# Performance work log

Measured on AMD Instinct MI355X. Metric: run time of the kernel, lower is better.

Reference implementation:

```python
import jax, jax.numpy as jnp
import numpy as np

B, S, D, H = 2, 2048, 2048, 16
HD = D // H  # head_dim = 128


def setup_inputs() -> dict:
    key = jax.random.key(0)
    ks = jax.random.split(key, 10)
    sc = 1.0 / np.sqrt(D)
    inp = {
        "hidden_states": jax.random.normal(ks[0], (B, S, D), dtype=jnp.float32),
        "attention_mask": jnp.zeros((B, 1, S, S), dtype=jnp.float32),
        "Wq": jax.random.normal(ks[1], (D, D), dtype=jnp.float32) * sc,
        "bq": jnp.zeros((D,), dtype=jnp.float32),
        "Wk": jax.random.normal(ks[2], (D, D), dtype=jnp.float32) * sc,
        "bk": jnp.zeros((D,), dtype=jnp.float32),
        "Wv": jax.random.normal(ks[3], (D, D), dtype=jnp.float32) * sc,
        "bv": jnp.zeros((D,), dtype=jnp.float32),
        "Wo": jax.random.normal(ks[4], (D, D), dtype=jnp.float32) * sc,
        "bo": jnp.zeros((D,), dtype=jnp.float32),
    }
    return inp


def reference(hidden_states, attention_mask, Wq, bq, Wk, bk, Wv, bv, Wo, bo):
    # torch Linear: y = x @ W^T + b
    q = hidden_states @ Wq.T + bq
    k = hidden_states @ Wk.T + bk
    v = hidden_states @ Wv.T + bv
    # [B,S,D] -> [B,H,S,HD]
    q = q.reshape(B, S, H, HD).transpose(0, 2, 1, 3)
    k = k.reshape(B, S, H, HD).transpose(0, 2, 1, 3)
    v = v.reshape(B, S, H, HD).transpose(0, 2, 1, 3)
    # RoPE in source is an identity passthrough; apply_rotary_pos_emb returns (q, k) unchanged.
    scores = jnp.einsum("bhqd,bhkd->bhqk", q, k) / jnp.sqrt(jnp.float32(HD))
    scores = scores + attention_mask  # broadcast over heads
    attn = jax.nn.softmax(scores, axis=-1)
    out = jnp.einsum("bhqk,bhkd->bhqd", attn, v)
    out = out.transpose(0, 2, 1, 3).reshape(B, S, D)
    return out @ Wo.T + bo
```

## Files before the change

### kernel.cpp

```cpp
#include <hip/hip_runtime.h>
#include <hip/hip_bf16.h>
#include <math.h>

typedef unsigned short u16;
typedef unsigned int u32;
typedef __attribute__((ext_vector_type(8))) short bf16x8;
typedef __attribute__((ext_vector_type(4))) float f32x4;

constexpr int Bc = 2, Sc = 2048, Dc = 2048, Hc = 16, HDc = 128;
constexpr int Mc = Bc * Sc;
constexpr float SCALE = 0.08838834764831845f;
constexpr float LOG2E = 1.4426950408889634f;

__device__ inline u16 f2bf(float f) {
  __hip_bfloat16 h = __float2bfloat16(f);
  return __builtin_bit_cast(u16, h);
}

typedef const __attribute__((address_space(1))) u32 glb_u32;
typedef __attribute__((address_space(3))) u32 lds_u32;
__device__ inline void gload16(const void* g, void* l) {
  __builtin_amdgcn_global_load_lds((glb_u32*)g, (lds_u32*)l, 16, 0, 0);
}

__global__ __launch_bounds__(256) void cvt5(
    const float* __restrict__ s0, u16* __restrict__ d0, int n0,
    const float* __restrict__ s1, u16* __restrict__ d1, int n1,
    const float* __restrict__ s2, u16* __restrict__ d2, int n2,
    const float* __restrict__ s3, u16* __restrict__ d3, int n3,
    const float* __restrict__ s4, u16* __restrict__ d4, int n4) {
  int i = blockIdx.x * 256 + threadIdx.x;
  const float* s; u16* d;
  if (i < n0) { s = s0; d = d0; }
  else { i -= n0;
    if (i < n1) { s = s1; d = d1; }
    else { i -= n1;
      if (i < n2) { s = s2; d = d2; }
      else { i -= n2;
        if (i < n3) { s = s3; d = d3; }
        else { i -= n3;
          if (i >= n4) return;
          s = s4; d = d4; } } } }
  float4 v = reinterpret_cast<const float4*>(s)[i];
  ushort4 o;
  o.x = f2bf(v.x); o.y = f2bf(v.y); o.z = f2bf(v.z); o.w = f2bf(v.w);
  reinterpret_cast<ushort4*>(d)[i] = o;
}

__global__ __launch_bounds__(512, 2) void qk_gemm8(
    const u16* __restrict__ A, const u16* __restrict__ Wq,
    const u16* __restrict__ Wk, const float* __restrict__ bq,
    const float* __restrict__ bk, u16* __restrict__ qout,
    u16* __restrict__ kout) {
  __shared__ u16 lds[65536];
  char* L = (char*)lds;
  const int t = threadIdx.x, w = t >> 6, lane = t & 63, g = lane >> 4, c = lane & 15;
  const int wm = w >> 2, wn = w & 3;
  const int m0 = blockIdx.y * 256, n0 = blockIdx.x * 256;
  const int z = blockIdx.z;
  const u16* W = z ? Wk : Wq;
  const float* bias = z ? bk : bq;
  const float scale = z ? 1.0f : SCALE * LOG2E;

  f32x4 acc[8][4];
#pragma unroll
  for (int m = 0; m < 8; ++m)
#pragma unroll
    for (int n = 0; n < 4; ++n) acc[m][n] = 0.f;

  const u16* sPtr[8];
  int dOff[8];
#pragma unroll
  for (int i = 0; i < 8; ++i) {
    int i2 = i & 3;
    int u = i2 * 512 + t;
    int row = u >> 3, p = u & 7;
    int cu = (p ^ row) & 7;
    const u16* base = (i < 4) ? (A + (size_t)(m0 + row) * Dc)
                              : (W + (size_t)(n0 + row) * Dc);
    sPtr[i] = base + cu * 8;
    dOff[i] = ((i >= 4) ? 32768 : 0) + (i2 >> 1) * 16384 +
              ((i2 & 1) * 512 + (t & 448)) * 16;
  }

  auto STAGE = [&](int d) {
#pragma unroll
    for (int i = 0; i < 8; ++i) {
      gload16(sPtr[i], L + d * 65536 + dOff[i]);
      sPtr[i] += 64;
    }
  };

  STAGE(0);
  asm volatile("s_waitcnt vmcnt(0)" ::: "memory");
  asm volatile("s_barrier" ::: "memory");

  int cur = 0;
  const char* AbBase = L + wm * 16384;
  const char* BbBase = L + 32768 + (wn >> 1) * 16384;
  const int rB0 = (wn & 1) * 64;

#pragma unroll 1
  for (int s = 0; s < 32; ++s) {
    if (s + 1 < 32) {
      STAGE(cur ^ 1);
      asm volatile("s_waitcnt vmcnt(8)" ::: "memory");
    } else {
      asm volatile("s_waitcnt vmcnt(0)" ::: "memory");
    }
    asm volatile("s_barrier" ::: "memory");

    const char* Ab = AbBase + cur * 65536;
    const char* Bb = BbBase + cur * 65536;
#pragma unroll
    for (int mh = 0; mh < 2; ++mh)
#pragma unroll
      for (int ks = 0; ks < 2; ++ks) {
        bf16x8 af[4], bf[4];
#pragma unroll
        for (int m4 = 0; m4 < 4; ++m4) {
          int row = (mh * 4 + m4) * 16 + c;
          af[m4] = *(const bf16x8*)(Ab + row * 128 + (((ks * 4 + g) ^ row) & 7) * 16);
        }
#pragma unroll
        for (int n = 0; n < 4; ++n) {
          int row = rB0 + n * 16 + c;
          bf[n] = *(const bf16x8*)(Bb + row * 128 + (((ks * 4 + g) ^ row) & 7) * 16);
        }
        __builtin_amdgcn_s_setprio(1);
#pragma unroll
        for (int m4 = 0; m4 < 4; ++m4)
#pragma unroll
          for (int n = 0; n < 4; ++n)
            acc[mh * 4 + m4][n] =
                __builtin_amdgcn_mfma_f32_16x16x32_bf16(af[m4], bf[n], acc[mh * 4 + m4][n], 0, 0, 0);
        __builtin_amdgcn_s_setprio(0);
      }

    asm volatile("s_barrier" ::: "memory");
    cur ^= 1;
  }

  u16* outp = z ? kout : qout;
#pragma unroll
  for (int n = 0; n < 4; ++n) {
    int col = n0 + wn * 64 + n * 16 + c;
    float bvv = bias[col];
    int h = col >> 7, d = col & (HDc - 1);
#pragma unroll
    for (int m = 0; m < 8; ++m)
#pragma unroll
      for (int r = 0; r < 4; ++r) {
        int row = m0 + wm * 128 + m * 16 + g * 4 + r;
        int b = row >> 11, si = row & (Sc - 1);
        outp[((size_t)((b * Hc + h) * Sc + si)) * HDc + d] =
            f2bf((acc[m][n][r] + bvv) * scale);
      }
  }
}

constexpr int GBM = 128, GBN = 128, GBK = 64;

__global__ __launch_bounds__(256) void v_gemm(
    const u16* __restrict__ A, const u16* __restrict__ W,
    const float* __restrict__ bias, u16* __restrict__ vout) {
  __shared__ u16 smem[17408];
  u16* As = smem;
  u16* Bs = smem + 8192;
  char* Asb = (char*)As;
  char* Bsb = (char*)Bs;
  const int t = threadIdx.x;
  const int w = t >> 6, lane = t & 63, g = lane >> 4, c = lane & 15;
  const int wm = w >> 1, wn = w & 1;
  const int m0 = blockIdx.y * GBM, n0 = blockIdx.x * GBN;

  f32x4 acc[4][4];
#pragma unroll
  for (int m = 0; m < 4; ++m)
#pragma unroll
    for (int n = 0; n < 4; ++n) acc[m][n] = 0.f;

  for (int k0 = 0; k0 < Dc; k0 += GBK) {
#pragma unroll
    for (int i = 0; i < 4; ++i) {
      int u = i * 256 + t;
      int row = u >> 3, p = u & 7;
      int cu = (p ^ row) & 7;
      int ub = i * 256 + (t & 192);
      gload16(A + (size_t)(m0 + row) * Dc + k0 + cu * 8, Asb + ub * 16);
      gload16(W + (size_t)(n0 + row) * Dc + k0 + cu * 8, Bsb + ub * 16);
    }
    __syncthreads();
#pragma unroll
    for (int s = 0; s < 2; ++s) {
      bf16x8 af[4], bfv[4];
#pragma unroll
      for (int m = 0; m < 4; ++m) {
        int row = wm * 64 + m * 16 + c;
        int scu = ((s * 4 + g) ^ row) & 7;
        af[m] = *(const bf16x8*)(Asb + row * 128 + scu * 16);
      }
#pragma unroll
      for (int n = 0; n < 4; ++n) {
        int row = wn * 64 + n * 16 + c;
        int scu = ((s * 4 + g) ^ row) & 7;
        bfv[n] = *(const bf16x8*)(Bsb + row * 128 + scu * 16);
      }
#pragma unroll
      for (int m = 0; m < 4; ++m)
#pragma unroll
        for (int n = 0; n < 4; ++n)
          acc[m][n] = __builtin_amdgcn_mfma_f32_16x16x32_bf16(af[m], bfv[n], acc[m][n], 0, 0, 0);
    }
    __syncthreads();
  }

  u16* CT = smem;
  __syncthreads();
#pragma unroll
  for (int m = 0; m < 4; ++m)
#pragma unroll
    for (int n = 0; n < 4; ++n) {
      int lcol = wn * 64 + n * 16 + c;
      float bvv = bias[n0 + lcol];
#pragma unroll
      for (int r = 0; r < 4; ++r) {
        int lrow = wm * 64 + m * 16 + g * 4 + r;
        CT[lcol * 136 + lrow] = f2bf(acc[m][n][r] + bvv);
      }
    }
  __syncthreads();
  const int b = m0 >> 11, h = n0 >> 7, s0 = m0 & (Sc - 1);
#pragma unroll
  for (int i = 0; i < 8; ++i) {
    int u = i * 256 + t;
    int d = u >> 4, su = u & 15;
    size_t gbase = ((size_t)((b * Hc + h) * HDc) + d) * Sc + s0;
#pragma unroll
    for (int p2 = 0; p2 < 4; ++p2) {
      int sl = su * 8 + p2 * 2;
      u32 val = (u32)CT[d * 136 + sl] | ((u32)CT[d * 136 + sl + 1] << 16);
      int w6 = sl & 63, blk = sl >> 6;
      int slot = ((w6 >> 5) << 5) | (((w6 >> 2) & 3) << 3) |
                 (((w6 >> 4) & 1) << 2) | (w6 & 3);
      *(u32*)&vout[gbase + blk * 64 + slot] = val;
    }
  }
}

__global__ __launch_bounds__(256) void gemm_out(
    const u16* __restrict__ A, const u16* __restrict__ W,
    const float* __restrict__ bias, float* __restrict__ outp) {
  __shared__ u16 smem[16384];
  u16* As = smem;
  u16* Bs = smem + 8192;
  char* Asb = (char*)As;
  char* Bsb = (char*)Bs;
  const int t = threadIdx.x;
  const int w = t >> 6, lane = t & 63, g = lane >> 4, c = lane & 15;
  const int wm = w >> 1, wn = w & 1;
  const int m0 = blockIdx.y * GBM, n0 = blockIdx.x * GBN;

  f32x4 acc[4][4];
#pragma unroll
  for (int m = 0; m < 4; ++m)
#pragma unroll
    for (int n = 0; n < 4; ++n) acc[m][n] = 0.f;

  for (int k0 = 0; k0 < Dc; k0 += GBK) {
#pragma unroll
    for (int i = 0; i < 4; ++i) {
      int u = i * 256 + t;
      int row = u >> 3, p = u & 7;
      int cu = (p ^ row) & 7;
      int ub = i * 256 + (t & 192);
      gload16(A + (size_t)(m0 + row) * Dc + k0 + cu * 8, Asb + ub * 16);
      gload16(W + (size_t)(n0 + row) * Dc + k0 + cu * 8, Bsb + ub * 16);
    }
    __syncthreads();
#pragma unroll
    for (int s = 0; s < 2; ++s) {
      bf16x8 af[4], bfv[4];
#pragma unroll
      for (int m = 0; m < 4; ++m) {
        int row = wm * 64 + m * 16 + c;
        int scu = ((s * 4 + g) ^ row) & 7;
        af[m] = *(const bf16x8*)(Asb + row * 128 + scu * 16);
      }
#pragma unroll
      for (int n = 0; n < 4; ++n) {
        int row = wn * 64 + n * 16 + c;
        int scu = ((s * 4 + g) ^ row) & 7;
        bfv[n] = *(const bf16x8*)(Bsb + row * 128 + scu * 16);
      }
#pragma unroll
      for (int m = 0; m < 4; ++m)
#pragma unroll
        for (int n = 0; n < 4; ++n)
          acc[m][n] = __builtin_amdgcn_mfma_f32_16x16x32_bf16(af[m], bfv[n], acc[m][n], 0, 0, 0);
    }
    __syncthreads();
  }

#pragma unroll
  for (int m = 0; m < 4; ++m)
#pragma unroll
    for (int n = 0; n < 4; ++n) {
      int col = n0 + wn * 64 + n * 16 + c;
      float bv = bias[col];
#pragma unroll
      for (int r = 0; r < 4; ++r) {
        int row = m0 + wm * 64 + m * 16 + g * 4 + r;
        outp[(size_t)row * Dc + col] = acc[m][n][r] + bv;
      }
    }
}

__global__ __launch_bounds__(128, 2) void attn_mfma(
    const u16* __restrict__ Q, const u16* __restrict__ K,
    const u16* __restrict__ VT, const float* __restrict__ mask,
    u16* __restrict__ outb) {
  __shared__ u16 Ks[64 * 128];
  __shared__ u16 Vt[128 * 64];
  char* Ksb = (char*)Ks;
  char* Vtb = (char*)Vt;
  const int t = threadIdx.x, w = t >> 6, lane = t & 63, g = lane >> 4, c = lane & 15;
  const int bid = blockIdx.x;
  const int nid = (bid & 7) * 128 + (bid >> 3);
  const int bh = nid >> 5;
  const int q0 = (nid & 31) * 64;
  const int bq = bh >> 4, h = bh & 15;
  const u16* Qp = Q + ((size_t)bh << 18);
  const u16* Kp = K + ((size_t)bh << 18);
  const u16* VTp = VT + ((size_t)bh << 18);

  bf16x8 qf0[4], qf1[4];
  {
    int qr0 = q0 + w * 32 + c;
#pragma unroll
    for (int d0 = 0; d0 < 4; ++d0) {
      qf0[d0] = *(const bf16x8*)(Qp + (size_t)qr0 * HDc + d0 * 32 + g * 8);
      qf1[d0] = *(const bf16x8*)(Qp + (size_t)(qr0 + 16) * HDc + d0 * 32 + g * 8);
    }
  }

  f32x4 po0[8], po1[8];
#pragma unroll
  for (int m = 0; m < 8; ++m) { po0[m] = 0.f; po1[m] = 0.f; }
  float lsum0 = 0.f, lsum1 = 0.f;
  const float* mrow0 = mask + ((size_t)bq * Sc + q0 + w * 32 + c) * Sc;
  const float* mrow1 = mrow0 + (size_t)16 * Sc;

#pragma unroll 1
  for (int kt = 0; kt < 32; ++kt) {
    const int k0 = kt * 64;
#pragma unroll
    for (int i = 0; i < 8; ++i) {
      int u = i * 128 + t, row = u >> 4, p = u & 15;
      int cu = (p & 8) | ((p ^ row) & 7);
      gload16(Kp + (size_t)(k0 + row) * HDc + cu * 8,
              Ksb + (i * 128 + (t & 64)) * 16);
    }
#pragma unroll
    for (int i = 0; i < 8; ++i) {
      int u = i * 128 + t, d = u >> 3, p = u & 7;
      int cu = (p ^ d) & 7;
      gload16(VTp + (size_t)d * Sc + k0 + cu * 8,
              Vtb + (i * 128 + (t & 64)) * 16);
    }
    float4 mk0[4], mk1[4];
#pragma unroll
    for (int n = 0; n < 4; ++n) {
      mk0[n] = *(const float4*)(mrow0 + k0 + n * 16 + g * 4);
      mk1[n] = *(const float4*)(mrow1 + k0 + n * 16 + g * 4);
    }
    __syncthreads();

    f32x4 sfr0[4], sfr1[4];
#pragma unroll
    for (int n = 0; n < 4; ++n) { sfr0[n] = 0.f; sfr1[n] = 0.f; }
    __builtin_amdgcn_s_setprio(1);
#pragma unroll
    for (int ds = 0; ds < 4; ++ds)
#pragma unroll
      for (int n = 0; n < 4; ++n) {
        int row = n * 16 + c;
        int cu = ds * 4 + g;
        int scu = (cu & 8) | ((cu ^ row) & 7);
        bf16x8 kf = *(const bf16x8*)(Ksb + row * 256 + scu * 16);
        sfr0[n] = __builtin_amdgcn_mfma_f32_16x16x32_bf16(kf, qf0[ds], sfr0[n], 0, 0, 0);
        sfr1[n] = __builtin_amdgcn_mfma_f32_16x16x32_bf16(kf, qf1[ds], sfr1[n], 0, 0, 0);
      }
    __builtin_amdgcn_s_setprio(0);

    u32 a01[4], a23[4], b01[4], b23[4];
#pragma unroll
    for (int n = 0; n < 4; ++n) {
      float p0 = __builtin_amdgcn_exp2f(fmaf(mk0[n].x, LOG2E, sfr0[n][0]));
      float p1 = __builtin_amdgcn_exp2f(fmaf(mk0[n].y, LOG2E, sfr0[n][1]));
      float p2 = __builtin_amdgcn_exp2f(fmaf(mk0[n].z, LOG2E, sfr0[n][2]));
      float p3 = __builtin_amdgcn_exp2f(fmaf(mk0[n].w, LOG2E, sfr0[n][3]));
      lsum0 += (p0 + p1) + (p2 + p3);
      a01[n] = (u32)f2bf(p0) | ((u32)f2bf(p1) << 16);
      a23[n] = (u32)f2bf(p2) | ((u32)f2bf(p3) << 16);
      float r0 = __builtin_amdgcn_exp2f(fmaf(mk1[n].x, LOG2E, sfr1[n][0]));
      float r1 = __builtin_amdgcn_exp2f(fmaf(mk1[n].y, LOG2E, sfr1[n][1]));
      float r2 = __builtin_amdgcn_exp2f(fmaf(mk1[n].z, LOG2E, sfr1[n][2]));
      float r3 = __builtin_amdgcn_exp2f(fmaf(mk1[n].w, LOG2E, sfr1[n][3]));
      lsum1 += (r0 + r1) + (r2 + r3);
      b01[n] = (u32)f2bf(r0) | ((u32)f2bf(r1) << 16);
      b23[n] = (u32)f2bf(r2) | ((u32)f2bf(r3) << 16);
    }

    __builtin_amdgcn_s_setprio(1);
#pragma unroll
    for (int s2 = 0; s2 < 2; ++s2) {
      uint4 pw0, pw1;
      pw0.x = a01[s2 * 2]; pw0.y = a23[s2 * 2];
      pw0.z = a01[s2 * 2 + 1]; pw0.w = a23[s2 * 2 + 1];
      pw1.x = b01[s2 * 2]; pw1.y = b23[s2 * 2];
      pw1.z = b01[s2 * 2 + 1]; pw1.w = b23[s2 * 2 + 1];
      bf16x8 pf0 = __builtin_bit_cast(bf16x8, pw0);
      bf16x8 pf1 = __builtin_bit_cast(bf16x8, pw1);
#pragma unroll
      for (int m = 0; m < 8; ++m) {
        int d = m * 16 + c;
        int scuv = ((s2 * 4 + g) ^ (d & 7)) & 7;
        bf16x8 vf = *(const bf16x8*)(Vtb + d * 128 + scuv * 16);
        po0[m] = __builtin_amdgcn_mfma_f32_16x16x32_bf16(vf, pf0, po0[m], 0, 0, 0);
        po1[m] = __builtin_amdgcn_mfma_f32_16x16x32_bf16(vf, pf1, po1[m], 0, 0, 0);
      }
    }
    __builtin_amdgcn_s_setprio(0);
    __syncthreads();
  }

  lsum0 += __shfl_xor(lsum0, 16, 64);
  lsum0 += __shfl_xor(lsum0, 32, 64);
  lsum1 += __shfl_xor(lsum1, 16, 64);
  lsum1 += __shfl_xor(lsum1, 32, 64);
  const float rl0 = 1.0f / lsum0;
  const float rl1 = 1.0f / lsum1;
  const int qg0 = q0 + w * 32 + c;
  u16* ob0 = outb + ((size_t)(bq * Sc + qg0)) * Dc + h * HDc;
  u16* ob1 = ob0 + (size_t)16 * Dc;
#pragma unroll
  for (int m = 0; m < 8; ++m) {
    ushort4 o4;
    o4.x = f2bf(po0[m][0] * rl0);
    o4.y = f2bf(po0[m][1] * rl0);
    o4.z = f2bf(po0[m][2] * rl0);
    o4.w = f2bf(po0[m][3] * rl0);
    *(ushort4*)(ob0 + m * 16 + g * 4) = o4;
    ushort4 o5;
    o5.x = f2bf(po1[m][0] * rl1);
    o5.y = f2bf(po1[m][1] * rl1);
    o5.z = f2bf(po1[m][2] * rl1);
    o5.w = f2bf(po1[m][3] * rl1);
    *(ushort4*)(ob1 + m * 16 + g * 4) = o5;
  }
}

extern "C" void kernel_launch(void* const* d_in, const int* in_sizes, int n_in,
                              void* d_out, int out_size, void* d_ws,
                              size_t ws_size, hipStream_t stream) {
  const float* hs   = (const float*)d_in[0];
  const float* mask = (const float*)d_in[1];
  const float* Wq   = (const float*)d_in[2];
  const float* bqp  = (const float*)d_in[3];
  const float* Wk   = (const float*)d_in[4];
  const float* bkp  = (const float*)d_in[5];
  const float* Wv   = (const float*)d_in[6];
  const float* bvp  = (const float*)d_in[7];
  const float* Wo   = (const float*)d_in[8];
  const float* bop  = (const float*)d_in[9];

  u16* Xb  = (u16*)d_ws;
  u16* Wqb = Xb + (size_t)Mc * Dc;
  u16* Wkb = Wqb + (size_t)Dc * Dc;
  u16* Wvb = Wkb + (size_t)Dc * Dc;
  u16* Wob = Wvb + (size_t)Dc * Dc;
  u16* qb  = Wob + (size_t)Dc * Dc;
  u16* kb  = qb + (size_t)Mc * Dc;
  u16* vtb = kb + (size_t)Mc * Dc;
  u16* ab  = vtb + (size_t)Mc * Dc;

  const int nh4 = Mc * Dc / 4;
  const int nw4 = Dc * Dc / 4;
  cvt5<<<dim3((nh4 + 4 * nw4) / 256), dim3(256), 0, stream>>>(
      hs, Xb, nh4, Wq, Wqb, nw4, Wk, Wkb, nw4, Wv, Wvb, nw4, Wo, Wob, nw4);

  qk_gemm8<<<dim3(Dc / 256, Mc / 256, 2), dim3(512), 0, stream>>>(
      Xb, Wqb, Wkb, bqp, bkp, qb, kb);
  v_gemm<<<dim3(Dc / GBN, Mc / GBM), dim3(256), 0, stream>>>(
      Xb, Wvb, bvp, vtb);
  attn_mfma<<<dim3(1024), dim3(128), 0, stream>>>(qb, kb, vtb, mask, ab);
  gemm_out<<<dim3(Dc / GBN, Mc / GBM), dim3(256), 0, stream>>>(
      ab, Wob, bop, (float*)d_out);
}
```

Baseline: 289.5 us.

## Double-buffer K/V tiles in attention and use 4-wave 128-query blocks

The attention kernel now uses 256 threads per block covering 128 queries, so each K/V tile loaded into LDS is shared by twice as many waves. K and V tiles are double-buffered and the next tile is prefetched while the current one is computed, with explicit vmcnt waits and barriers replacing __syncthreads. The aim is to hide global-to-LDS load latency and halve K/V reload traffic. In exchange LDS per block doubles to 64KB, which lowers occupancy, and the hand-counted vmcnt values must match the loads actually in flight, including the mask loads.

Result: faster. 282.8 us (median of 2 runs) (-2.3%).

```diff
diff --git a/kernel.cpp b/kernel.cpp
--- a/kernel.cpp
+++ b/kernel.cpp
@@ -316,24 +316,51 @@
     }
 }
 
-__global__ __launch_bounds__(128, 2) void attn_mfma(
+__global__ __launch_bounds__(256) void attn_mfma(
     const u16* __restrict__ Q, const u16* __restrict__ K,
     const u16* __restrict__ VT, const float* __restrict__ mask,
     u16* __restrict__ outb) {
-  __shared__ u16 Ks[64 * 128];
-  __shared__ u16 Vt[128 * 64];
-  char* Ksb = (char*)Ks;
-  char* Vtb = (char*)Vt;
+  __shared__ u16 Ks[2][64 * 128];
+  __shared__ u16 Vt[2][64 * 128];
   const int t = threadIdx.x, w = t >> 6, lane = t & 63, g = lane >> 4, c = lane & 15;
   const int bid = blockIdx.x;
-  const int nid = (bid & 7) * 128 + (bid >> 3);
-  const int bh = nid >> 5;
-  const int q0 = (nid & 31) * 64;
+  const int nid = (bid & 7) * 64 + (bid >> 3);
+  const int bh = nid >> 4;
+  const int q0 = (nid & 15) * 128;
   const int bq = bh >> 4, h = bh & 15;
   const u16* Qp = Q + ((size_t)bh << 18);
   const u16* Kp = K + ((size_t)bh << 18);
   const u16* VTp = VT + ((size_t)bh << 18);
 
+  const u16* kSrc[4];
+  const u16* vSrc[4];
+  int kOff[4], vOff[4];
+#pragma unroll
+  for (int i = 0; i < 4; ++i) {
+    int u = i * 256 + t;
+    int row = u >> 4, p = u & 15;
+    int cu = (p & 8) | ((p ^ row) & 7);
+    kSrc[i] = Kp + (size_t)row * HDc + cu * 8;
+    kOff[i] = (i * 256 + (t & 192)) * 16;
+    int d = u >> 3, pv = u & 7;
+    int cv = (pv ^ d) & 7;
+    vSrc[i] = VTp + (size_t)d * Sc + cv * 8;
+    vOff[i] = (i * 256 + (t & 192)) * 16;
+  }
+
+  auto STAGE = [&](int buf) {
+#pragma unroll
+    for (int i = 0; i < 4; ++i) {
+      gload16(kSrc[i], (char*)Ks[buf] + kOff[i]);
+      kSrc[i] += 64 * HDc;
+    }
+#pragma unroll
+    for (int i = 0; i < 4; ++i) {
+      gload16(vSrc[i], (char*)Vt[buf] + vOff[i]);
+      vSrc[i] += 64;
+    }
+  };
+
   bf16x8 qf0[4], qf1[4];
   {
     int qr0 = q0 + w * 32 + c;
@@ -351,30 +378,30 @@
   const float* mrow0 = mask + ((size_t)bq * Sc + q0 + w * 32 + c) * Sc;
   const float* mrow1 = mrow0 + (size_t)16 * Sc;
 
+  STAGE(0);
+  asm volatile("s_waitcnt vmcnt(0)" ::: "memory");
+  asm volatile("s_barrier" ::: "memory");
+  int cur = 0;
+
 #pragma unroll 1
   for (int kt = 0; kt < 32; ++kt) {
     const int k0 = kt * 64;
-#pragma unroll
-    for (int i = 0; i < 8; ++i) {
-      int u = i * 128 + t, row = u >> 4, p = u & 15;
-      int cu = (p & 8) | ((p ^ row) & 7);
-      gload16(Kp + (size_t)(k0 + row) * HDc + cu * 8,
-              Ksb + (i * 128 + (t & 64)) * 16);
-    }
-#pragma unroll
-    for (int i = 0; i < 8; ++i) {
-      int u = i * 128 + t, d = u >> 3, p = u & 7;
-      int cu = (p ^ d) & 7;
-      gload16(VTp + (size_t)d * Sc + k0 + cu * 8,
-              Vtb + (i * 128 + (t & 64)) * 16);
-    }
     float4 mk0[4], mk1[4];
 #pragma unroll
     for (int n = 0; n < 4; ++n) {
       mk0[n] = *(const float4*)(mrow0 + k0 + n * 16 + g * 4);
       mk1[n] = *(const float4*)(mrow1 + k0 + n * 16 + g * 4);
     }
-    __syncthreads();
+    if (kt + 1 < 32) {
+      STAGE(cur ^ 1);
+      asm volatile("s_waitcnt vmcnt(16)" ::: "memory");
+    } else {
+      asm volatile("s_waitcnt vmcnt(8)" ::: "memory");
+    }
+    asm volatile("s_barrier" ::: "memory");
+
+    const char* Ksb = (const char*)Ks[cur];
+    const char* Vtb = (const char*)Vt[cur];
 
     f32x4 sfr0[4], sfr1[4];
 #pragma unroll
@@ -432,7 +459,8 @@
       }
     }
     __builtin_amdgcn_s_setprio(0);
-    __syncthreads();
+    asm volatile("s_barrier" ::: "memory");
+    cur ^= 1;
   }
 
   lsum0 += __shfl_xor(lsum0, 16, 64);
@@ -494,7 +522,7 @@
       Xb, Wqb, Wkb, bqp, bkp, qb, kb);
   v_gemm<<<dim3(Dc / GBN, Mc / GBM), dim3(256), 0, stream>>>(
       Xb, Wvb, bvp, vtb);
-  attn_mfma<<<dim3(1024), dim3(128), 0, stream>>>(qb, kb, vtb, mask, ab);
+  attn_mfma<<<dim3(512), dim3(256), 0, stream>>>(qb, kb, vtb, mask, ab);
   gemm_out<<<dim3(Dc / GBN, Mc / GBM), dim3(256), 0, stream>>>(
       ab, Wob, bop, (float*)d_out);
 }
```
